# Performance work log

Hardware: AMD Instinct MI355X
Metric: run time of the kernel (lower is better)

The kernel has to match this reference:

```python
import jax, jax.numpy as jnp
import numpy as np

B, T, C = 4, 1024, 1024
H = 16
DH = C // H  # 64


def setup_inputs() -> dict:
    key = jax.random.key(0)
    ks = jax.random.split(key, 10)
    s = 0.02
    return {
        "x": jax.random.normal(ks[0], (B, T, C), dtype=jnp.float32),
        "Wq": jax.random.normal(ks[1], (C, C), dtype=jnp.float32) * s,
        "bq": jnp.zeros((C,), dtype=jnp.float32),
        "Wk": jax.random.normal(ks[2], (C, C), dtype=jnp.float32) * s,
        "bk": jnp.zeros((C,), dtype=jnp.float32),
        "Wv": jax.random.normal(ks[3], (C, C), dtype=jnp.float32) * s,
        "bv": jnp.zeros((C,), dtype=jnp.float32),
        "Wp": jax.random.normal(ks[4], (C, C), dtype=jnp.float32) * s,
        "bp": jnp.zeros((C,), dtype=jnp.float32),
    }


def reference(x, Wq, bq, Wk, bk, Wv, bv, Wp, bp):
    b, t, c = x.shape
    # QKV projections, split into heads: [b, H, t, DH]
    def heads(y):
        return y.reshape(b, t, H, DH).transpose(0, 2, 1, 3)
    q = heads(x @ Wq + bq)
    k = heads(x @ Wk + bk)
    v = heads(x @ Wv + bv)
    # Causal attention. Original masks with -inf BEFORE scaling; -inf*scale is
    # still -inf, so mask-then-scale == scale-then-mask.
    scores = jnp.einsum("bhqd,bhkd->bhqk", q, k) * (DH ** -0.5)
    causal = jnp.tril(jnp.ones((t, t), dtype=bool))
    scores = jnp.where(causal, scores, -jnp.inf)
    attn = jax.nn.softmax(scores, axis=-1)  # dropout p=0.0 -> identity
    ctx = jnp.einsum("bhqk,bhkd->bhqd", attn, v)
    ctx = ctx.transpose(0, 2, 1, 3).reshape(b, t, c)
    return ctx @ Wp + bp
```

## Files before the change

kernel.cpp:

```cpp
#include <hip/hip_runtime.h>


typedef unsigned short ushort_t;
typedef __attribute__((ext_vector_type(8))) __bf16 bf16x8;
typedef __attribute__((ext_vector_type(8))) unsigned short us8;
typedef __attribute__((ext_vector_type(4))) unsigned short us4;
typedef __attribute__((ext_vector_type(4))) float f32x4;

#define AS1 __attribute__((address_space(1)))
#define AS3 __attribute__((address_space(3)))

__device__ __forceinline__ ushort_t f2bf(float f) {
  unsigned int u = __float_as_uint(f);
  u += 0x7fffu + ((u >> 16) & 1u);
  return (ushort_t)(u >> 16);
}


__global__ void cvt_x_kernel(const float* __restrict__ x, ushort_t* __restrict__ xb) {
  const int i = blockIdx.x * 256 + threadIdx.x;
  const float4 v = reinterpret_cast<const float4*>(x)[i];
  us4 o;
  o.x = f2bf(v.x); o.y = f2bf(v.y); o.z = f2bf(v.z); o.w = f2bf(v.w);
  reinterpret_cast<us4*>(xb)[i] = o;
}

__global__ void cvt_w4_kernel(const float* __restrict__ Wq, const float* __restrict__ Wk,
                              const float* __restrict__ Wv, const float* __restrict__ Wp,
                              ushort_t* __restrict__ WQKVT, ushort_t* __restrict__ WPT) {
  __shared__ float t[32][33];
  const int z = blockIdx.z;
  const float* W = (z == 0) ? Wq : (z == 1) ? Wk : (z == 2) ? Wv : Wp;
  ushort_t* Wt = (z == 3) ? WPT : (WQKVT + ((size_t)z << 20));
  const float wscale = (z == 0) ? 0.125f : 1.0f;
  const int n0 = blockIdx.x * 32, k0 = blockIdx.y * 32;
  const int tx = threadIdx.x, ty = threadIdx.y;
#pragma unroll
  for (int i = ty; i < 32; i += 8)
    t[i][tx] = W[(size_t)(k0 + i) * 1024 + n0 + tx];
  __syncthreads();
#pragma unroll
  for (int i = ty; i < 32; i += 8)
    Wt[(size_t)(n0 + i) * 1024 + k0 + tx] = f2bf(t[tx][i] * wscale);
}


__global__ __launch_bounds__(512, 2) void gemm_qkv256_kernel(
    const ushort_t* __restrict__ A, const ushort_t* __restrict__ Bt,
    const float* __restrict__ bq, const float* __restrict__ bk,
    const float* __restrict__ bv, ushort_t* __restrict__ QKVB,
    ushort_t* __restrict__ VT) {
  __shared__ ushort_t smem[2][2][256 * 32];
  const int tid = threadIdx.x;
  const int wave = tid >> 6, lane = tid & 63;
  const int lgrp = lane >> 4, lmod = lane & 15;
  const int wr = wave >> 2, wc = wave & 3;
  const int swz = (blockIdx.x & 7) * 24 + (blockIdx.x >> 3);
  const int row0 = (swz / 12) * 256, col0 = (swz % 12) * 256;

  const ushort_t* Ag = A + (size_t)row0 * 1024;
  const ushort_t* Bg = Bt + (size_t)col0 * 1024;

  auto stage8k = [&](ushort_t* reg, const ushort_t* g0, int i) {
    const int row = i * 128 + wave * 16 + (lane >> 2);
    const int cb = (lane & 3) << 4;
    __builtin_amdgcn_global_load_lds(
        (AS1 void*)(g0 + (size_t)row * 1024 + (cb >> 1)),
        (AS3 void*)((char*)reg + i * 8192 + wave * 1024), 16, 0, 0);
  };

  f32x4 acc[8][4] = {};
  constexpr int nt = 32;

  stage8k(&smem[0][0][0], Ag, 0);
  stage8k(&smem[0][0][0], Ag, 1);
  stage8k(&smem[0][1][0], Bg, 0);
  stage8k(&smem[0][1][0], Bg, 1);

  for (int t = 0; t < nt; ++t) {
    const int cur = t & 1, nxt = cur ^ 1;
    const char* curA = (const char*)&smem[cur][0][0];
    const char* curB = (const char*)&smem[cur][1][0];
    if (t + 1 < nt) {
      stage8k(&smem[nxt][0][0], Ag + (t + 1) * 32, 0);
      stage8k(&smem[nxt][0][0], Ag + (t + 1) * 32, 1);
      asm volatile("s_waitcnt vmcnt(2)" ::: "memory");
    } else {
      asm volatile("s_waitcnt vmcnt(0)" ::: "memory");
    }
    __builtin_amdgcn_sched_barrier(0);
    __builtin_amdgcn_s_barrier();

    bf16x8 bfr[4], af[4];
#pragma unroll
    for (int ni = 0; ni < 4; ++ni)
      bfr[ni] = *reinterpret_cast<const bf16x8*>(
          curB + (wc * 64 + ni * 16 + lmod) * 64 + lgrp * 16);
#pragma unroll
    for (int mi = 0; mi < 4; ++mi)
      af[mi] = *reinterpret_cast<const bf16x8*>(
          curA + (wr * 128 + mi * 16 + lmod) * 64 + lgrp * 16);
    if (t + 1 < nt) {
      stage8k(&smem[nxt][1][0], Bg + (t + 1) * 32, 0);
      stage8k(&smem[nxt][1][0], Bg + (t + 1) * 32, 1);
    }
    __builtin_amdgcn_s_setprio(1);
#pragma unroll
    for (int mi = 0; mi < 4; ++mi)
#pragma unroll
      for (int ni = 0; ni < 4; ++ni)
        acc[mi][ni] = __builtin_amdgcn_mfma_f32_16x16x32_bf16(af[mi], bfr[ni], acc[mi][ni], 0, 0, 0);
    __builtin_amdgcn_s_setprio(0);
    __builtin_amdgcn_s_barrier();

#pragma unroll
    for (int mi = 0; mi < 4; ++mi)
      af[mi] = *reinterpret_cast<const bf16x8*>(
          curA + (wr * 128 + (4 + mi) * 16 + lmod) * 64 + lgrp * 16);
    __builtin_amdgcn_s_setprio(1);
#pragma unroll
    for (int mi = 0; mi < 4; ++mi)
#pragma unroll
      for (int ni = 0; ni < 4; ++ni)
        acc[4 + mi][ni] = __builtin_amdgcn_mfma_f32_16x16x32_bf16(af[mi], bfr[ni], acc[4 + mi][ni], 0, 0, 0);
    __builtin_amdgcn_s_setprio(0);
    __builtin_amdgcn_s_barrier();
  }

  if (col0 < 2048) {
    const float* bsel = (col0 < 1024) ? bq : bk;
    const float bsc = (col0 < 1024) ? 0.125f : 1.0f;
    float bvv[4];
#pragma unroll
    for (int ni = 0; ni < 4; ++ni)
      bvv[ni] = bsel[(col0 & 1023) + wc * 64 + ni * 16 + lmod] * bsc;
#pragma unroll
    for (int mi = 0; mi < 8; ++mi) {
#pragma unroll
      for (int ni = 0; ni < 4; ++ni) {
        const int col = col0 + wc * 64 + ni * 16 + lmod;
#pragma unroll
        for (int r = 0; r < 4; ++r) {
          const int row = row0 + wr * 128 + mi * 16 + lgrp * 4 + r;
          QKVB[(size_t)row * 3072 + col] = f2bf(acc[mi][ni][r] + bvv[ni]);
        }
      }
    }
  } else {
    float bvv[4];
#pragma unroll
    for (int ni = 0; ni < 4; ++ni)
      bvv[ni] = bv[(col0 - 2048) + wc * 64 + ni * 16 + lmod];
#pragma unroll
    for (int mi = 0; mi < 8; ++mi) {
#pragma unroll
      for (int ni = 0; ni < 4; ++ni) {
        const int hd = (col0 - 2048) + wc * 64 + ni * 16 + lmod;
        const int R = row0 + wr * 128 + mi * 16 + lgrp * 4;
        const int bb = R >> 10, tl = R & 1023;
        us4 o;
#pragma unroll
        for (int r = 0; r < 4; ++r) o[r] = f2bf(acc[mi][ni][r] + bvv[ni]);
        *reinterpret_cast<us4*>(VT + ((size_t)(bb * 16 + (hd >> 6)) * 64 + (hd & 63)) * 1024 + tl) = o;
      }
    }
  }
}


__global__ __launch_bounds__(256, 2) void gemm_proj_kernel(
    const ushort_t* __restrict__ A, const ushort_t* __restrict__ Bt,
    const float* __restrict__ bias, float* __restrict__ Cout) {
  constexpr int BM = 64, WR = 32, MFR = 2, NIT = 3;
  __shared__ ushort_t As[BM * 32];
  __shared__ ushort_t Bs[128 * 32];
  const int tid = threadIdx.x;
  const int wave = tid >> 6, lane = tid & 63;
  const int lgrp = lane >> 4, lmod = lane & 15;
  const int wr = wave >> 1, wc = wave & 1;
  const int cpx = gridDim.x >> 3;
  const int swz = (blockIdx.x & 7) * cpx + (blockIdx.x >> 3);
  const int row0 = (swz / 8) * BM, col0 = (swz % 8) * 128;

  f32x4 acc[MFR][4] = {};

  for (int k0 = 0; k0 < 1024; k0 += 32) {
#pragma unroll
    for (int it = 0; it < NIT; ++it) {
      const int c0 = it * 256 + wave * 64;
      const int c = c0 + lane;
      if (c0 < BM * 4) {
        const int r = c >> 2, kk = (c & 3) << 3;
        __builtin_amdgcn_global_load_lds(
            (AS1 void*)(A + (size_t)(row0 + r) * 1024 + k0 + kk),
            (AS3 void*)(As + (c0 << 3)), 16, 0, 0);
      } else {
        const int cb = c - BM * 4;
        const int r = cb >> 2, kk = (cb & 3) << 3;
        __builtin_amdgcn_global_load_lds(
            (AS1 void*)(Bt + (size_t)(col0 + r) * 1024 + k0 + kk),
            (AS3 void*)(Bs + ((c0 - BM * 4) << 3)), 16, 0, 0);
      }
    }
    __syncthreads();

    bf16x8 af[MFR], bfr[4];
#pragma unroll
    for (int i = 0; i < MFR; ++i)
      af[i] = *reinterpret_cast<const bf16x8*>(&As[(wr * WR + i * 16 + lmod) * 32 + lgrp * 8]);
#pragma unroll
    for (int i = 0; i < 4; ++i)
      bfr[i] = *reinterpret_cast<const bf16x8*>(&Bs[(wc * 64 + i * 16 + lmod) * 32 + lgrp * 8]);
    __builtin_amdgcn_s_setprio(1);
#pragma unroll
    for (int mi = 0; mi < MFR; ++mi)
#pragma unroll
      for (int ni = 0; ni < 4; ++ni)
        acc[mi][ni] = __builtin_amdgcn_mfma_f32_16x16x32_bf16(af[mi], bfr[ni], acc[mi][ni], 0, 0, 0);
    __builtin_amdgcn_s_setprio(0);
    __syncthreads();
  }

  float bvv[4];
#pragma unroll
  for (int ni = 0; ni < 4; ++ni) bvv[ni] = bias[col0 + wc * 64 + ni * 16 + lmod];
#pragma unroll
  for (int mi = 0; mi < MFR; ++mi)
#pragma unroll
    for (int ni = 0; ni < 4; ++ni) {
      const int col = col0 + wc * 64 + ni * 16 + lmod;
#pragma unroll
      for (int r = 0; r < 4; ++r) {
        const int row = row0 + wr * WR + mi * 16 + lgrp * 4 + r;
        Cout[(size_t)row * 1024 + col] = acc[mi][ni][r] + bvv[ni];
      }
    }
}


__global__ __launch_bounds__(256, 2) void attn_kernel(
    const ushort_t* __restrict__ QKV, const ushort_t* __restrict__ VT,
    ushort_t* __restrict__ Og) {
  const int bid = blockIdx.x;
  const int swz = (bid & 7) * 64 + (bid >> 3);
  const int p = swz & 7, bh = swz >> 3;
  const int b = bh >> 4, h = bh & 15;
  const int jmax = 15 - p;
  const int tid = threadIdx.x;
  const int wave = tid >> 6, lane = tid & 63;
  const int lgrp = lane >> 4, lmod = lane & 15;

  __shared__ ushort_t Ks[64 * 72];
  __shared__ ushort_t Vs[64 * 72];
  __shared__ ushort_t Ps[4][16 * 72];

  const size_t xrow0 = (size_t)b * 1024;
  const int qlo = p * 64 + wave * 16;
  const int qhi = jmax * 64 + wave * 16;

  bf16x8 qfl[2], qfh[2];
#pragma unroll
  for (int ks = 0; ks < 2; ++ks) {
    qfl[ks] = *reinterpret_cast<const bf16x8*>(
        QKV + (xrow0 + qlo + lmod) * 3072 + h * 64 + ks * 32 + lgrp * 8);
    qfh[ks] = *reinterpret_cast<const bf16x8*>(
        QKV + (xrow0 + qhi + lmod) * 3072 + h * 64 + ks * 32 + lgrp * 8);
  }

  f32x4 ol[4] = {}, oh[4] = {};
  float ll[4] = {0.f, 0.f, 0.f, 0.f}, lh[4] = {0.f, 0.f, 0.f, 0.f};

  const int sr = tid >> 3;
  const int scc = (tid & 7) << 3;
  us8 kreg0, kreg1, vreg0, vreg1;

  auto load_tile = [&](int j) {
    const ushort_t* kp = QKV + (xrow0 + j * 64 + sr) * 3072 + 1024 + h * 64 + scc;
    kreg0 = *reinterpret_cast<const us8*>(kp);
    kreg1 = *reinterpret_cast<const us8*>(kp + 32 * 3072);
    const ushort_t* vp = VT + ((size_t)bh * 64 + sr) * 1024 + j * 64 + scc;
    vreg0 = *reinterpret_cast<const us8*>(vp);
    vreg1 = *reinterpret_cast<const us8*>(vp + 32 * 1024);
  };
  auto write_tile = [&]() {
    *reinterpret_cast<us8*>(&Ks[sr * 72 + scc]) = kreg0;
    *reinterpret_cast<us8*>(&Ks[(32 + sr) * 72 + scc]) = kreg1;
    *reinterpret_cast<us8*>(&Vs[sr * 72 + scc]) = vreg0;
    *reinterpret_cast<us8*>(&Vs[(32 + sr) * 72 + scc]) = vreg1;
  };

  auto step = [&](const bf16x8* qf, f32x4* oacc, float* lsum, bool diag) {
    f32x4 s[4];
    __builtin_amdgcn_s_setprio(1);
#pragma unroll
    for (int cg = 0; cg < 4; ++cg) {
      f32x4 a = {};
#pragma unroll
      for (int ks = 0; ks < 2; ++ks) {
        bf16x8 kf = *reinterpret_cast<const bf16x8*>(
            &Ks[(cg * 16 + lmod) * 72 + ks * 32 + lgrp * 8]);
        a = __builtin_amdgcn_mfma_f32_16x16x32_bf16(qf[ks], kf, a, 0, 0, 0);
      }
      s[cg] = a;
    }
    __builtin_amdgcn_s_setprio(0);
    if (diag) {
      const int qloc = wave * 16 + lgrp * 4;
#pragma unroll
      for (int cg = 0; cg < 4; ++cg) {
        const int kcol = cg * 16 + lmod;
#pragma unroll
        for (int r = 0; r < 4; ++r)
          if (kcol > qloc + r) s[cg][r] = -1e30f;
      }
    }
#pragma unroll
    for (int cg = 0; cg < 4; ++cg)
#pragma unroll
      for (int r = 0; r < 4; ++r) s[cg][r] = __expf(s[cg][r]);
#pragma unroll
    for (int r = 0; r < 4; ++r)
      lsum[r] += (s[0][r] + s[1][r]) + (s[2][r] + s[3][r]);
#pragma unroll
    for (int cg = 0; cg < 4; ++cg)
#pragma unroll
      for (int r = 0; r < 4; ++r)
        Ps[wave][(lgrp * 4 + r) * 72 + cg * 16 + lmod] = f2bf(s[cg][r]);
    __builtin_amdgcn_s_setprio(1);
#pragma unroll
    for (int ks = 0; ks < 2; ++ks) {
      bf16x8 pf = *reinterpret_cast<const bf16x8*>(
          &Ps[wave][lmod * 72 + ks * 32 + lgrp * 8]);
#pragma unroll
      for (int dhg = 0; dhg < 4; ++dhg) {
        bf16x8 vf = *reinterpret_cast<const bf16x8*>(
            &Vs[(dhg * 16 + lmod) * 72 + ks * 32 + lgrp * 8]);
        oacc[dhg] = __builtin_amdgcn_mfma_f32_16x16x32_bf16(pf, vf, oacc[dhg], 0, 0, 0);
      }
    }
    __builtin_amdgcn_s_setprio(0);
  };

  load_tile(0);
  for (int j = 0; j <= jmax; ++j) {
    __syncthreads();
    write_tile();
    __syncthreads();
    if (j < jmax) load_tile(j + 1);
    if (j <= p) step(qfl, ol, ll, j == p);
    step(qfh, oh, lh, j == jmax);
  }

#pragma unroll
  for (int m = 1; m <= 8; m <<= 1)
#pragma unroll
    for (int r = 0; r < 4; ++r) {
      ll[r] += __shfl_xor(ll[r], m);
      lh[r] += __shfl_xor(lh[r], m);
    }

#pragma unroll
  for (int dhg = 0; dhg < 4; ++dhg) {
    const int col = h * 64 + dhg * 16 + lmod;
#pragma unroll
    for (int r = 0; r < 4; ++r) {
      Og[(xrow0 + qlo + lgrp * 4 + r) * 1024 + col] = f2bf(ol[dhg][r] / ll[r]);
      Og[(xrow0 + qhi + lgrp * 4 + r) * 1024 + col] = f2bf(oh[dhg][r] / lh[r]);
    }
  }
}


extern "C" void kernel_launch(void* const* d_in, const int* in_sizes, int n_in,
                              void* d_out, int out_size, void* d_ws, size_t ws_size,
                              hipStream_t stream) {
  const float* x  = (const float*)d_in[0];
  const float* Wq = (const float*)d_in[1];
  const float* bq = (const float*)d_in[2];
  const float* Wk = (const float*)d_in[3];
  const float* bk = (const float*)d_in[4];
  const float* Wv = (const float*)d_in[5];
  const float* bv = (const float*)d_in[6];
  const float* Wp = (const float*)d_in[7];
  const float* bp = (const float*)d_in[8];
  float* out = (float*)d_out;

  char* ws = (char*)d_ws;
  ushort_t* XB    = (ushort_t*)(ws);
  ushort_t* WQKVT = (ushort_t*)(ws + ( 8ull << 20));
  ushort_t* WPT   = (ushort_t*)(ws + (14ull << 20));
  ushort_t* QKVB  = (ushort_t*)(ws + (16ull << 20));
  ushort_t* VT    = (ushort_t*)(ws + (40ull << 20));

  cvt_x_kernel<<<4096, 256, 0, stream>>>(x, XB);
  cvt_w4_kernel<<<dim3(32, 32, 4), dim3(32, 8), 0, stream>>>(Wq, Wk, Wv, Wp, WQKVT, WPT);
  gemm_qkv256_kernel<<<192, 512, 0, stream>>>(XB, WQKVT, bq, bk, bv, QKVB, VT);
  attn_kernel<<<512, 256, 0, stream>>>(QKVB, VT, XB);
  gemm_proj_kernel<<<512, 256, 0, stream>>>(XB, WPT, bp, out);
}
```

Before: 98.40 us.

## Retile QKV GEMM to 128x128 with swizzled BK=64 LDS and vectorized epilogues

```diff
diff --git a/kernel.cpp b/kernel.cpp
--- a/kernel.cpp
+++ b/kernel.cpp
@@ -14,6 +14,12 @@
   unsigned int u = __float_as_uint(f);
   u += 0x7fffu + ((u >> 16) & 1u);
   return (ushort_t)(u >> 16);
+}
+
+__device__ __forceinline__ ushort_t f2bf_hw(float f) {
+  union { __bf16 b; ushort_t u; } cv;
+  cv.b = (__bf16)f;
+  return cv.u;
 }
 
 
@@ -45,196 +51,205 @@
 }
 
 
-__global__ __launch_bounds__(512, 2) void gemm_qkv256_kernel(
+__global__ __launch_bounds__(256, 3) void gemm_qkv128_kernel(
     const ushort_t* __restrict__ A, const ushort_t* __restrict__ Bt,
     const float* __restrict__ bq, const float* __restrict__ bk,
     const float* __restrict__ bv, ushort_t* __restrict__ QKVB,
     ushort_t* __restrict__ VT) {
-  __shared__ ushort_t smem[2][2][256 * 32];
-  const int tid = threadIdx.x;
-  const int wave = tid >> 6, lane = tid & 63;
-  const int lgrp = lane >> 4, lmod = lane & 15;
-  const int wr = wave >> 2, wc = wave & 3;
-  const int swz = (blockIdx.x & 7) * 24 + (blockIdx.x >> 3);
-  const int row0 = (swz / 12) * 256, col0 = (swz % 12) * 256;
-
-  const ushort_t* Ag = A + (size_t)row0 * 1024;
-  const ushort_t* Bg = Bt + (size_t)col0 * 1024;
-
-  auto stage8k = [&](ushort_t* reg, const ushort_t* g0, int i) {
-    const int row = i * 128 + wave * 16 + (lane >> 2);
-    const int cb = (lane & 3) << 4;
-    __builtin_amdgcn_global_load_lds(
-        (AS1 void*)(g0 + (size_t)row * 1024 + (cb >> 1)),
-        (AS3 void*)((char*)reg + i * 8192 + wave * 1024), 16, 0, 0);
-  };
-
-  f32x4 acc[8][4] = {};
-  constexpr int nt = 32;
-
-  stage8k(&smem[0][0][0], Ag, 0);
-  stage8k(&smem[0][0][0], Ag, 1);
-  stage8k(&smem[0][1][0], Bg, 0);
-  stage8k(&smem[0][1][0], Bg, 1);
-
-  for (int t = 0; t < nt; ++t) {
-    const int cur = t & 1, nxt = cur ^ 1;
-    const char* curA = (const char*)&smem[cur][0][0];
-    const char* curB = (const char*)&smem[cur][1][0];
-    if (t + 1 < nt) {
-      stage8k(&smem[nxt][0][0], Ag + (t + 1) * 32, 0);
-      stage8k(&smem[nxt][0][0], Ag + (t + 1) * 32, 1);
-      asm volatile("s_waitcnt vmcnt(2)" ::: "memory");
-    } else {
-      asm volatile("s_waitcnt vmcnt(0)" ::: "memory");
-    }
-    __builtin_amdgcn_sched_barrier(0);
-    __builtin_amdgcn_s_barrier();
-
-    bf16x8 bfr[4], af[4];
-#pragma unroll
-    for (int ni = 0; ni < 4; ++ni)
-      bfr[ni] = *reinterpret_cast<const bf16x8*>(
-          curB + (wc * 64 + ni * 16 + lmod) * 64 + lgrp * 16);
-#pragma unroll
-    for (int mi = 0; mi < 4; ++mi)
-      af[mi] = *reinterpret_cast<const bf16x8*>(
-          curA + (wr * 128 + mi * 16 + lmod) * 64 + lgrp * 16);
-    if (t + 1 < nt) {
-      stage8k(&smem[nxt][1][0], Bg + (t + 1) * 32, 0);
-      stage8k(&smem[nxt][1][0], Bg + (t + 1) * 32, 1);
-    }
-    __builtin_amdgcn_s_setprio(1);
-#pragma unroll
-    for (int mi = 0; mi < 4; ++mi)
-#pragma unroll
-      for (int ni = 0; ni < 4; ++ni)
-        acc[mi][ni] = __builtin_amdgcn_mfma_f32_16x16x32_bf16(af[mi], bfr[ni], acc[mi][ni], 0, 0, 0);
-    __builtin_amdgcn_s_setprio(0);
-    __builtin_amdgcn_s_barrier();
-
-#pragma unroll
-    for (int mi = 0; mi < 4; ++mi)
-      af[mi] = *reinterpret_cast<const bf16x8*>(
-          curA + (wr * 128 + (4 + mi) * 16 + lmod) * 64 + lgrp * 16);
-    __builtin_amdgcn_s_setprio(1);
-#pragma unroll
-    for (int mi = 0; mi < 4; ++mi)
-#pragma unroll
-      for (int ni = 0; ni < 4; ++ni)
-        acc[4 + mi][ni] = __builtin_amdgcn_mfma_f32_16x16x32_bf16(af[mi], bfr[ni], acc[4 + mi][ni], 0, 0, 0);
-    __builtin_amdgcn_s_setprio(0);
-    __builtin_amdgcn_s_barrier();
-  }
-
-  if (col0 < 2048) {
-    const float* bsel = (col0 < 1024) ? bq : bk;
-    const float bsc = (col0 < 1024) ? 0.125f : 1.0f;
-    float bvv[4];
-#pragma unroll
-    for (int ni = 0; ni < 4; ++ni)
-      bvv[ni] = bsel[(col0 & 1023) + wc * 64 + ni * 16 + lmod] * bsc;
-#pragma unroll
-    for (int mi = 0; mi < 8; ++mi) {
-#pragma unroll
-      for (int ni = 0; ni < 4; ++ni) {
-        const int col = col0 + wc * 64 + ni * 16 + lmod;
-#pragma unroll
-        for (int r = 0; r < 4; ++r) {
-          const int row = row0 + wr * 128 + mi * 16 + lgrp * 4 + r;
-          QKVB[(size_t)row * 3072 + col] = f2bf(acc[mi][ni][r] + bvv[ni]);
-        }
-      }
-    }
-  } else {
-    float bvv[4];
-#pragma unroll
-    for (int ni = 0; ni < 4; ++ni)
-      bvv[ni] = bv[(col0 - 2048) + wc * 64 + ni * 16 + lmod];
-#pragma unroll
-    for (int mi = 0; mi < 8; ++mi) {
-#pragma unroll
-      for (int ni = 0; ni < 4; ++ni) {
-        const int hd = (col0 - 2048) + wc * 64 + ni * 16 + lmod;
-        const int R = row0 + wr * 128 + mi * 16 + lgrp * 4;
-        const int bb = R >> 10, tl = R & 1023;
-        us4 o;
-#pragma unroll
-        for (int r = 0; r < 4; ++r) o[r] = f2bf(acc[mi][ni][r] + bvv[ni]);
-        *reinterpret_cast<us4*>(VT + ((size_t)(bb * 16 + (hd >> 6)) * 64 + (hd & 63)) * 1024 + tl) = o;
-      }
-    }
-  }
-}
-
-
-__global__ __launch_bounds__(256, 2) void gemm_proj_kernel(
-    const ushort_t* __restrict__ A, const ushort_t* __restrict__ Bt,
-    const float* __restrict__ bias, float* __restrict__ Cout) {
-  constexpr int BM = 64, WR = 32, MFR = 2, NIT = 3;
-  __shared__ ushort_t As[BM * 32];
-  __shared__ ushort_t Bs[128 * 32];
+  __shared__ ushort_t As[128 * 64];
+  __shared__ ushort_t Bs[128 * 64];
   const int tid = threadIdx.x;
   const int wave = tid >> 6, lane = tid & 63;
   const int lgrp = lane >> 4, lmod = lane & 15;
   const int wr = wave >> 1, wc = wave & 1;
-  const int cpx = gridDim.x >> 3;
-  const int swz = (blockIdx.x & 7) * cpx + (blockIdx.x >> 3);
-  const int row0 = (swz / 8) * BM, col0 = (swz % 8) * 128;
-
-  f32x4 acc[MFR][4] = {};
-
-  for (int k0 = 0; k0 < 1024; k0 += 32) {
-#pragma unroll
-    for (int it = 0; it < NIT; ++it) {
-      const int c0 = it * 256 + wave * 64;
-      const int c = c0 + lane;
-      if (c0 < BM * 4) {
-        const int r = c >> 2, kk = (c & 3) << 3;
-        __builtin_amdgcn_global_load_lds(
-            (AS1 void*)(A + (size_t)(row0 + r) * 1024 + k0 + kk),
-            (AS3 void*)(As + (c0 << 3)), 16, 0, 0);
-      } else {
-        const int cb = c - BM * 4;
-        const int r = cb >> 2, kk = (cb & 3) << 3;
-        __builtin_amdgcn_global_load_lds(
-            (AS1 void*)(Bt + (size_t)(col0 + r) * 1024 + k0 + kk),
-            (AS3 void*)(Bs + ((c0 - BM * 4) << 3)), 16, 0, 0);
+  const int swz = (blockIdx.x & 7) * 96 + (blockIdx.x >> 3);
+  const int rowt = swz / 24, colt = swz % 24;
+  const int row0 = rowt * 128, col0 = colt * 128;
+  const bool isV = (colt >= 16);
+
+  const int sslot = (tid & 7) ^ ((tid >> 3) & 7);
+  const int srow = tid >> 3;
+
+  auto stage = [&](int t) {
+    const ushort_t* Asrc = A + (size_t)row0 * 1024 + t * 64 + sslot * 8;
+    const ushort_t* Bsrc = Bt + (size_t)col0 * 1024 + t * 64 + sslot * 8;
+#pragma unroll
+    for (int i = 0; i < 4; ++i) {
+      __builtin_amdgcn_global_load_lds(
+          (AS1 void*)(Asrc + (size_t)(i * 32 + srow) * 1024),
+          (AS3 void*)(As + (i * 256 + wave * 64) * 8), 16, 0, 0);
+      __builtin_amdgcn_global_load_lds(
+          (AS1 void*)(Bsrc + (size_t)(i * 32 + srow) * 1024),
+          (AS3 void*)(Bs + (i * 256 + wave * 64) * 8), 16, 0, 0);
+    }
+  };
+
+  f32x4 acc[4][4] = {};
+  const int xm = lmod & 7;
+
+  for (int t = 0; t < 16; ++t) {
+    stage(t);
+    asm volatile("s_waitcnt vmcnt(0)" ::: "memory");
+    __builtin_amdgcn_s_barrier();
+
+    bf16x8 af[4][2], bfr[4][2];
+#pragma unroll
+    for (int mi = 0; mi < 4; ++mi)
+#pragma unroll
+      for (int ks = 0; ks < 2; ++ks)
+        af[mi][ks] = *reinterpret_cast<const bf16x8*>(
+            &As[(wr * 64 + mi * 16 + lmod) * 64 + (((ks << 2) | lgrp) ^ xm) * 8]);
+#pragma unroll
+    for (int ni = 0; ni < 4; ++ni)
+#pragma unroll
+      for (int ks = 0; ks < 2; ++ks)
+        bfr[ni][ks] = *reinterpret_cast<const bf16x8*>(
+            &Bs[(wc * 64 + ni * 16 + lmod) * 64 + (((ks << 2) | lgrp) ^ xm) * 8]);
+
+    __builtin_amdgcn_s_setprio(1);
+    if (!isV) {
+#pragma unroll
+      for (int mi = 0; mi < 4; ++mi)
+#pragma unroll
+        for (int ni = 0; ni < 4; ++ni)
+#pragma unroll
+          for (int ks = 0; ks < 2; ++ks)
+            acc[mi][ni] = __builtin_amdgcn_mfma_f32_16x16x32_bf16(
+                bfr[ni][ks], af[mi][ks], acc[mi][ni], 0, 0, 0);
+    } else {
+#pragma unroll
+      for (int mi = 0; mi < 4; ++mi)
+#pragma unroll
+        for (int ni = 0; ni < 4; ++ni)
+#pragma unroll
+          for (int ks = 0; ks < 2; ++ks)
+            acc[mi][ni] = __builtin_amdgcn_mfma_f32_16x16x32_bf16(
+                af[mi][ks], bfr[ni][ks], acc[mi][ni], 0, 0, 0);
+    }
+    __builtin_amdgcn_s_setprio(0);
+    __builtin_amdgcn_s_barrier();
+  }
+
+  if (!isV) {
+    const float* bsel = (col0 < 1024) ? bq : bk;
+    const float bsc = (col0 < 1024) ? 0.125f : 1.0f;
+#pragma unroll
+    for (int ni = 0; ni < 4; ++ni) {
+      const int colb = wc * 64 + ni * 16 + lgrp * 4;
+      const float4 bb = *reinterpret_cast<const float4*>(&bsel[(col0 & 1023) + colb]);
+#pragma unroll
+      for (int mi = 0; mi < 4; ++mi) {
+        const int row = row0 + wr * 64 + mi * 16 + lmod;
+        us4 o;
+        o.x = f2bf(acc[mi][ni][0] + bb.x * bsc);
+        o.y = f2bf(acc[mi][ni][1] + bb.y * bsc);
+        o.z = f2bf(acc[mi][ni][2] + bb.z * bsc);
+        o.w = f2bf(acc[mi][ni][3] + bb.w * bsc);
+        *reinterpret_cast<us4*>(&QKVB[(size_t)row * 3072 + col0 + colb]) = o;
       }
     }
-    __syncthreads();
-
-    bf16x8 af[MFR], bfr[4];
-#pragma unroll
-    for (int i = 0; i < MFR; ++i)
-      af[i] = *reinterpret_cast<const bf16x8*>(&As[(wr * WR + i * 16 + lmod) * 32 + lgrp * 8]);
+  } else {
+    float bvv[4];
+#pragma unroll
+    for (int ni = 0; ni < 4; ++ni)
+      bvv[ni] = bv[(col0 - 2048) + wc * 64 + ni * 16 + lmod];
+#pragma unroll
+    for (int mi = 0; mi < 4; ++mi) {
+#pragma unroll
+      for (int ni = 0; ni < 4; ++ni) {
+        const int hd = (col0 - 2048) + wc * 64 + ni * 16 + lmod;
+        const int R = row0 + wr * 64 + mi * 16 + lgrp * 4;
+        const int bb = R >> 10, tl = R & 1023;
+        us4 o;
+#pragma unroll
+        for (int r = 0; r < 4; ++r) o[r] = f2bf(acc[mi][ni][r] + bvv[ni]);
+        *reinterpret_cast<us4*>(VT + ((size_t)(bb * 16 + (hd >> 6)) * 64 + (hd & 63)) * 1024 + tl) = o;
+      }
+    }
+  }
+}
+
+
+__global__ __launch_bounds__(256, 3) void gemm_proj_kernel(
+    const ushort_t* __restrict__ A, const ushort_t* __restrict__ Bt,
+    const float* __restrict__ bias, float* __restrict__ Cout) {
+  __shared__ ushort_t As[64 * 64];
+  __shared__ ushort_t Bs[128 * 64];
+  const int tid = threadIdx.x;
+  const int wave = tid >> 6, lane = tid & 63;
+  const int lgrp = lane >> 4, lmod = lane & 15;
+  const int wr = wave >> 1, wc = wave & 1;
+  const int swz = (blockIdx.x & 7) * 64 + (blockIdx.x >> 3);
+  const int row0 = (swz >> 3) * 64, col0 = (swz & 7) * 128;
+
+  const int sslot = (tid & 7) ^ ((tid >> 3) & 7);
+  const int srow = tid >> 3;
+
+  auto stage = [&](int t) {
+    const ushort_t* Asrc = A + (size_t)row0 * 1024 + t * 64 + sslot * 8;
+    const ushort_t* Bsrc = Bt + (size_t)col0 * 1024 + t * 64 + sslot * 8;
+#pragma unroll
+    for (int i = 0; i < 2; ++i)
+      __builtin_amdgcn_global_load_lds(
+          (AS1 void*)(Asrc + (size_t)(i * 32 + srow) * 1024),
+          (AS3 void*)(As + (i * 256 + wave * 64) * 8), 16, 0, 0);
 #pragma unroll
     for (int i = 0; i < 4; ++i)
-      bfr[i] = *reinterpret_cast<const bf16x8*>(&Bs[(wc * 64 + i * 16 + lmod) * 32 + lgrp * 8]);
+      __builtin_amdgcn_global_load_lds(
+          (AS1 void*)(Bsrc + (size_t)(i * 32 + srow) * 1024),
+          (AS3 void*)(Bs + (i * 256 + wave * 64) * 8), 16, 0, 0);
+  };
+
+  f32x4 acc[2][4] = {};
+  const int xm = lmod & 7;
+
+  for (int t = 0; t < 16; ++t) {
+    stage(t);
+    asm volatile("s_waitcnt vmcnt(0)" ::: "memory");
+    __builtin_amdgcn_s_barrier();
+
+    bf16x8 af[2][2], bfr[4][2];
+#pragma unroll
+    for (int mi = 0; mi < 2; ++mi)
+#pragma unroll
+      for (int ks = 0; ks < 2; ++ks)
+        af[mi][ks] = *reinterpret_cast<const bf16x8*>(
+            &As[(wr * 32 + mi * 16 + lmod) * 64 + (((ks << 2) | lgrp) ^ xm) * 8]);
+#pragma unroll
+    for (int ni = 0; ni < 4; ++ni)
+#pragma unroll
+      for (int ks = 0; ks < 2; ++ks)
+        bfr[ni][ks] = *reinterpret_cast<const bf16x8*>(
+            &Bs[(wc * 64 + ni * 16 + lmod) * 64 + (((ks << 2) | lgrp) ^ xm) * 8]);
+
     __builtin_amdgcn_s_setprio(1);
 #pragma unroll
-    for (int mi = 0; mi < MFR; ++mi)
+    for (int mi = 0; mi < 2; ++mi)
 #pragma unroll
       for (int ni = 0; ni < 4; ++ni)
-        acc[mi][ni] = __builtin_amdgcn_mfma_f32_16x16x32_bf16(af[mi], bfr[ni], acc[mi][ni], 0, 0, 0);
+#pragma unroll
+        for (int ks = 0; ks < 2; ++ks)
+          acc[mi][ni] = __builtin_amdgcn_mfma_f32_16x16x32_bf16(
+              bfr[ni][ks], af[mi][ks], acc[mi][ni], 0, 0, 0);
     __builtin_amdgcn_s_setprio(0);
-    __syncthreads();
-  }
-
-  float bvv[4];
-#pragma unroll
-  for (int ni = 0; ni < 4; ++ni) bvv[ni] = bias[col0 + wc * 64 + ni * 16 + lmod];
-#pragma unroll
-  for (int mi = 0; mi < MFR; ++mi)
-#pragma unroll
-    for (int ni = 0; ni < 4; ++ni) {
-      const int col = col0 + wc * 64 + ni * 16 + lmod;
-#pragma unroll
-      for (int r = 0; r < 4; ++r) {
-        const int row = row0 + wr * WR + mi * 16 + lgrp * 4 + r;
-        Cout[(size_t)row * 1024 + col] = acc[mi][ni][r] + bvv[ni];
-      }
-    }
+    __builtin_amdgcn_s_barrier();
+  }
+
+#pragma unroll
+  for (int ni = 0; ni < 4; ++ni) {
+    const int colb = col0 + wc * 64 + ni * 16 + lgrp * 4;
+    const float4 bb = *reinterpret_cast<const float4*>(&bias[colb]);
+#pragma unroll
+    for (int mi = 0; mi < 2; ++mi) {
+      const int row = row0 + wr * 32 + mi * 16 + lmod;
+      float4 o;
+      o.x = acc[mi][ni][0] + bb.x;
+      o.y = acc[mi][ni][1] + bb.y;
+      o.z = acc[mi][ni][2] + bb.z;
+      o.w = acc[mi][ni][3] + bb.w;
+      *reinterpret_cast<float4*>(&Cout[(size_t)row * 1024 + colb]) = o;
+    }
+  }
 }
 
 
@@ -325,7 +340,7 @@
     for (int cg = 0; cg < 4; ++cg)
 #pragma unroll
       for (int r = 0; r < 4; ++r)
-        Ps[wave][(lgrp * 4 + r) * 72 + cg * 16 + lmod] = f2bf(s[cg][r]);
+        Ps[wave][(lgrp * 4 + r) * 72 + cg * 16 + lmod] = f2bf_hw(s[cg][r]);
     __builtin_amdgcn_s_setprio(1);
 #pragma unroll
     for (int ks = 0; ks < 2; ++ks) {
@@ -364,8 +379,8 @@
     const int col = h * 64 + dhg * 16 + lmod;
 #pragma unroll
     for (int r = 0; r < 4; ++r) {
-      Og[(xrow0 + qlo + lgrp * 4 + r) * 1024 + col] = f2bf(ol[dhg][r] / ll[r]);
-      Og[(xrow0 + qhi + lgrp * 4 + r) * 1024 + col] = f2bf(oh[dhg][r] / lh[r]);
+      Og[(xrow0 + qlo + lgrp * 4 + r) * 1024 + col] = f2bf_hw(ol[dhg][r] / ll[r]);
+      Og[(xrow0 + qhi + lgrp * 4 + r) * 1024 + col] = f2bf_hw(oh[dhg][r] / lh[r]);
     }
   }
 }
@@ -394,7 +409,7 @@
 
   cvt_x_kernel<<<4096, 256, 0, stream>>>(x, XB);
   cvt_w4_kernel<<<dim3(32, 32, 4), dim3(32, 8), 0, stream>>>(Wq, Wk, Wv, Wp, WQKVT, WPT);
-  gemm_qkv256_kernel<<<192, 512, 0, stream>>>(XB, WQKVT, bq, bk, bv, QKVB, VT);
+  gemm_qkv128_kernel<<<768, 256, 0, stream>>>(XB, WQKVT, bq, bk, bv, QKVB, VT);
   attn_kernel<<<512, 256, 0, stream>>>(QKVB, VT, XB);
   gemm_proj_kernel<<<512, 256, 0, stream>>>(XB, WPT, bp, out);
 }
```

After: 186.4 us. 89.4% more time.
